# Optimization experiments

Measured on AMD Instinct MI355X. Metric: run time of the kernel, lower is better.

The kernel has to match this reference:

```python
import jax, jax.numpy as jnp
import numpy as np

N_EXPERTS = 8
TOP_K = 2


def setup_inputs() -> dict:
    key = jax.random.key(0)
    ks = jax.random.split(key, 5)
    B, T, C, E, H = 8, 2048, 256, 8, 682  # H = int(8/3*256)
    scale = 1.0 / np.sqrt(C)
    return {
        "x": jax.random.normal(ks[0], (B, T, C), dtype=jnp.float32),
        "router_w": jax.random.normal(ks[1], (E, C), dtype=jnp.float32) * scale,
        "w1": jax.random.normal(ks[2], (E, H, C), dtype=jnp.float32) * scale,
        "w2": jax.random.normal(ks[3], (E, C, H), dtype=jnp.float32) * (1.0 / np.sqrt(H)),
        "w3": jax.random.normal(ks[4], (E, H, C), dtype=jnp.float32) * scale,
    }


def reference(x, router_w, w1, w2, w3):
    B, T, C = x.shape
    flat = x.reshape(-1, C)  # [N, C]

    # Router: softmax over experts, top-k selection, renormalize.
    logits = flat @ router_w.T                     # [N, E]
    probs = jax.nn.softmax(logits, axis=-1)
    topk_probs, topk_idx = jax.lax.top_k(probs, TOP_K)
    topk_probs = topk_probs / (jnp.sum(topk_probs, axis=-1, keepdims=True) + 1e-9)

    # Dense gate matrix [N, E]: zero for non-selected experts (same math as
    # the masked loop, since unselected experts contribute weight 0).
    onehot = jax.nn.one_hot(topk_idx, N_EXPERTS, dtype=flat.dtype)  # [N, K, E]
    gates = jnp.einsum("nk,nke->ne", topk_probs, onehot)           # [N, E]

    # SwiGLU experts, computed densely over E and combined with gates.
    h1 = jnp.einsum("nc,ehc->neh", flat, w1)       # [N, E, H]
    h3 = jnp.einsum("nc,ehc->neh", flat, w3)       # [N, E, H]
    h = jax.nn.silu(h1) * h3                       # [N, E, H]
    y = jnp.einsum("neh,ech->nec", h, w2)          # [N, E, C]
    out = jnp.einsum("ne,nec->nc", gates, y)       # [N, C]
    return out.reshape(B, T, C)
```

## Files before the change

kernel.cpp:

```cpp
#include <hip/hip_runtime.h>
#include <hip/hip_bf16.h>

#define N_TOK 16384
#define C_DIM 256
#define E_NUM 8
#define H_DIM 682
#define H_PAD 768
#define NROWS (N_TOK * 2)
#define HB 64
#define APB (NROWS / HB)

typedef short short8 __attribute__((ext_vector_type(8)));
typedef float floatx4 __attribute__((ext_vector_type(4)));
typedef unsigned int uint;

__device__ inline unsigned short f2bf(float v) {
    union { float f; uint u; } x; x.f = v;
    uint r = (x.u + 0x7fffu + ((x.u >> 16) & 1u)) >> 16;
    return (unsigned short)r;
}
__device__ inline float bf2f(unsigned short v) {
    union { uint u; float f; } x; x.u = ((uint)v) << 16; return x.f;
}

__device__ __forceinline__ void load_lds16(const void* g, void* l) {
    __builtin_amdgcn_global_load_lds(
        (const __attribute__((address_space(1))) unsigned int*)g,
        (__attribute__((address_space(3))) unsigned int*)l, 16, 0, 0);
}

#define P13 (E_NUM * H_PAD * (C_DIM / 2))
#define P2  (E_NUM * C_DIM * (H_PAD / 2))
__global__ void wconvert(const float* __restrict__ w1, const float* __restrict__ w3,
                         const float* __restrict__ w2, unsigned short* __restrict__ w1b,
                         unsigned short* __restrict__ w3b, unsigned short* __restrict__ w2b) {
    int idx = blockIdx.x * 256 + threadIdx.x;
    if (idx < 2 * P13) {
        const float* src = (idx < P13) ? w1 : w3;
        unsigned short* dst = (idx < P13) ? w1b : w3b;
        int i = (idx < P13) ? idx : idx - P13;
        int e = i / (H_PAD * (C_DIM / 2));
        int rem = i - e * (H_PAD * (C_DIM / 2));
        int r = rem / (C_DIM / 2);
        int c2 = rem - r * (C_DIM / 2);
        uint v = 0;
        if (r < H_DIM) {
            const float2 f = *(const float2*)(src + ((size_t)e * H_DIM + r) * C_DIM + c2 * 2);
            v = (uint)f2bf(f.x) | ((uint)f2bf(f.y) << 16);
        }
        ((uint*)dst)[i] = v;
    } else if (idx < 2 * P13 + P2) {
        int i = idx - 2 * P13;
        int e = i / (C_DIM * (H_PAD / 2));
        int rem = i - e * (C_DIM * (H_PAD / 2));
        int r = rem / (H_PAD / 2);
        int c2 = rem - r * (H_PAD / 2);
        uint v = 0;
        if (c2 * 2 < H_DIM) {
            const float2 f = *(const float2*)(w2 + ((size_t)e * C_DIM + r) * H_DIM + c2 * 2);
            v = (uint)f2bf(f.x) | ((uint)f2bf(f.y) << 16);
        }
        ((uint*)w2b)[i] = v;
    }
}

__global__ __launch_bounds__(256) void router_kernel(
    const float* __restrict__ x, const float* __restrict__ rw,
    unsigned short* __restrict__ xb, int* __restrict__ as_e, float* __restrict__ as_gate) {
    __shared__ float rws[E_NUM * C_DIM];
    int tid = threadIdx.x;
    for (int i = tid; i < E_NUM * C_DIM; i += 256) rws[i] = rw[i];
    __syncthreads();
    int wave = tid >> 6, lane = tid & 63;
    int t = blockIdx.x * 4 + wave;
    const float4 xv = *(const float4*)(x + (size_t)t * C_DIM + lane * 4);
    uint2 pk;
    pk.x = (uint)f2bf(xv.x) | ((uint)f2bf(xv.y) << 16);
    pk.y = (uint)f2bf(xv.z) | ((uint)f2bf(xv.w) << 16);
    *(uint2*)(xb + (size_t)t * C_DIM + lane * 4) = pk;
    float p[E_NUM];
#pragma unroll
    for (int e = 0; e < E_NUM; e++) {
        const float* wr = &rws[e * C_DIM + lane * 4];
        p[e] = xv.x * wr[0] + xv.y * wr[1] + xv.z * wr[2] + xv.w * wr[3];
    }
#pragma unroll
    for (int off = 32; off >= 1; off >>= 1) {
#pragma unroll
        for (int e = 0; e < E_NUM; e++) p[e] += __shfl_down(p[e], off, 64);
    }
    if (lane == 0) {
        float m = p[0];
#pragma unroll
        for (int e = 1; e < E_NUM; e++) m = fmaxf(m, p[e]);
        float s = 0.f, q[E_NUM];
#pragma unroll
        for (int e = 0; e < E_NUM; e++) { q[e] = expf(p[e] - m); s += q[e]; }
#pragma unroll
        for (int e = 0; e < E_NUM; e++) q[e] /= s;
        int e0 = 0;
#pragma unroll
        for (int e = 1; e < E_NUM; e++) if (q[e] > q[e0]) e0 = e;
        int e1 = (e0 == 0) ? 1 : 0;
#pragma unroll
        for (int e = 0; e < E_NUM; e++) {
            if (e != e0 && q[e] > q[e1]) e1 = e;
        }
        float g0 = q[e0], g1 = q[e1];
        float denom = g0 + g1 + 1e-9f;
        g0 /= denom; g1 /= denom;
        as_e[t * 2] = e0; as_gate[t * 2] = g0;
        as_e[t * 2 + 1] = e1; as_gate[t * 2 + 1] = g1;
    }
}

__global__ __launch_bounds__(256) void hist_kernel(const int* __restrict__ as_e,
                                                   int* __restrict__ block_hist) {
    __shared__ int lh[E_NUM];
    int b = blockIdx.x, tid = threadIdx.x;
    if (tid < E_NUM) lh[tid] = 0;
    __syncthreads();
    for (int i = tid; i < APB; i += 256) atomicAdd(&lh[as_e[b * APB + i]], 1);
    __syncthreads();
    if (tid < E_NUM) block_hist[b * E_NUM + tid] = lh[tid];
}

__global__ void scan2_kernel(const int* __restrict__ block_hist, int* __restrict__ offsets,
                             int* __restrict__ block_base) {
    __shared__ int tot[E_NUM], off[E_NUM];
    int e = threadIdx.x;
    if (e < E_NUM) {
        int s = 0;
        for (int b = 0; b < HB; b++) s += block_hist[b * E_NUM + e];
        tot[e] = s;
    }
    __syncthreads();
    if (e == 0) {
        int acc = 0;
        for (int i = 0; i < E_NUM; i++) { off[i] = acc; offsets[i] = acc; acc += tot[i]; }
        offsets[E_NUM] = acc;
    }
    __syncthreads();
    if (e < E_NUM) {
        int acc = off[e];
        for (int b = 0; b < HB; b++) { block_base[b * E_NUM + e] = acc; acc += block_hist[b * E_NUM + e]; }
    }
}

__global__ __launch_bounds__(256) void scatter_kernel(
    const int* __restrict__ as_e, const int* __restrict__ block_base,
    int* __restrict__ row_token, int* __restrict__ as_row) {
    __shared__ int cur[E_NUM];
    int b = blockIdx.x, tid = threadIdx.x;
    if (tid < E_NUM) cur[tid] = block_base[b * E_NUM + tid];
    __syncthreads();
    for (int i = tid; i < APB; i += 256) {
        int a = b * APB + i;
        int e = as_e[a];
        int p = atomicAdd(&cur[e], 1);
        row_token[p] = a >> 1;
        as_row[a] = p;
    }
}

__global__ __launch_bounds__(256, 2) void expert_ffn1(
    const unsigned short* __restrict__ xb, const unsigned short* __restrict__ w1b,
    const unsigned short* __restrict__ w3b, const int* __restrict__ offsets,
    const int* __restrict__ row_token, unsigned short* __restrict__ h) {
    int e = blockIdx.x >> 6;
    int mt = blockIdx.x & 63;
    int c = blockIdx.y;
    int off0 = offsets[e], off1 = offsets[e + 1];
    int row0 = off0 + mt * 128;
    if (row0 >= off1) return;
    int mval = min(128, off1 - row0);

    __shared__ union {
        struct { unsigned short A[128 * 32], B1[128 * 32], B3[128 * 32]; } s;
        unsigned short Hs[128 * 136];
    } sm;

    int tid = threadIdx.x, lane = tid & 63, w = tid >> 6;
    int wm = w & 1, wn = w >> 1;
    int ra = tid >> 2;
    int acol = (tid & 3) * 8;
    int tok0 = row_token[row0 + min(ra, mval - 1)];
    int tok1 = row_token[row0 + min(ra + 64, mval - 1)];
    const unsigned short* a0p = xb + (size_t)tok0 * C_DIM + acol;
    const unsigned short* a1p = xb + (size_t)tok1 * C_DIM + acol;
    const unsigned short* b1p0 = w1b + ((size_t)e * H_PAD + c * 128 + ra) * C_DIM + acol;
    const unsigned short* b1p1 = b1p0 + (size_t)64 * C_DIM;
    const unsigned short* b3p0 = w3b + ((size_t)e * H_PAD + c * 128 + ra) * C_DIM + acol;
    const unsigned short* b3p1 = b3p0 + (size_t)64 * C_DIM;

    unsigned short* ldsA0 = sm.s.A + w * 512;
    unsigned short* ldsA1 = sm.s.A + 2048 + w * 512;
    unsigned short* ldsB10 = sm.s.B1 + w * 512;
    unsigned short* ldsB11 = sm.s.B1 + 2048 + w * 512;
    unsigned short* ldsB30 = sm.s.B3 + w * 512;
    unsigned short* ldsB31 = sm.s.B3 + 2048 + w * 512;

    int ko = (lane >> 4) * 8;
    int l15 = lane & 15;
    int arowf = wm * 64 + l15;
    int browf = wn * 64 + l15;
    int quad = lane >> 4;

    floatx4 acc1[4][4], acc3[4][4];
#pragma unroll
    for (int m = 0; m < 4; m++)
#pragma unroll
        for (int n = 0; n < 4; n++) {
            acc1[m][n] = (floatx4){0.f, 0.f, 0.f, 0.f};
            acc3[m][n] = (floatx4){0.f, 0.f, 0.f, 0.f};
        }

    for (int kt = 0; kt < 8; kt++) {
        int kb = kt * 32;
        load_lds16(a0p + kb, ldsA0);
        load_lds16(a1p + kb, ldsA1);
        load_lds16(b1p0 + kb, ldsB10);
        load_lds16(b1p1 + kb, ldsB11);
        load_lds16(b3p0 + kb, ldsB30);
        load_lds16(b3p1 + kb, ldsB31);
        __syncthreads();
        short8 af[4], b1f[4], b3f[4];
#pragma unroll
        for (int m = 0; m < 4; m++) af[m] = *(short8*)&sm.s.A[(arowf + m * 16) * 32 + ko];
#pragma unroll
        for (int n = 0; n < 4; n++) {
            b1f[n] = *(short8*)&sm.s.B1[(browf + n * 16) * 32 + ko];
            b3f[n] = *(short8*)&sm.s.B3[(browf + n * 16) * 32 + ko];
        }
#pragma unroll
        for (int m = 0; m < 4; m++)
#pragma unroll
            for (int n = 0; n < 4; n++) {
                acc1[m][n] = __builtin_amdgcn_mfma_f32_16x16x32_bf16(af[m], b1f[n], acc1[m][n], 0, 0, 0);
                acc3[m][n] = __builtin_amdgcn_mfma_f32_16x16x32_bf16(af[m], b3f[n], acc3[m][n], 0, 0, 0);
            }
        __syncthreads();
    }

#pragma unroll
    for (int m = 0; m < 4; m++)
#pragma unroll
        for (int n = 0; n < 4; n++)
#pragma unroll
            for (int r = 0; r < 4; r++) {
                float h1 = acc1[m][n][r], h3 = acc3[m][n][r];
                float sv = h1 / (1.0f + __expf(-h1)) * h3;
                sm.Hs[(wm * 64 + m * 16 + quad * 4 + r) * 136 + wn * 64 + n * 16 + l15] = f2bf(sv);
            }
    __syncthreads();
#pragma unroll
    for (int it = 0; it < 8; it++) {
        int s = it * 256 + tid;
        int row = s >> 4, c16 = s & 15;
        if (row < mval)
            *(int4*)(h + (size_t)(row0 + row) * H_PAD + c * 128 + c16 * 8) =
                *(int4*)&sm.Hs[row * 136 + c16 * 8];
    }
}

__global__ __launch_bounds__(256, 2) void expert_ffn2(
    const unsigned short* __restrict__ h, const unsigned short* __restrict__ w2b,
    const int* __restrict__ offsets, unsigned short* __restrict__ y) {
    int e = blockIdx.x >> 6;
    int mt = blockIdx.x & 63;
    int p = blockIdx.y;
    int off0 = offsets[e], off1 = offsets[e + 1];
    int row0 = off0 + mt * 128;
    if (row0 >= off1) return;
    int mval = min(128, off1 - row0);

    __shared__ union {
        struct { unsigned short A[128 * 32], B[128 * 32]; } s;
        unsigned short Hs[128 * 136];
    } sm;

    int tid = threadIdx.x, lane = tid & 63, w = tid >> 6;
    int wm = w & 1, wn = w >> 1;
    int ra = tid >> 2;
    int acol = (tid & 3) * 8;
    const unsigned short* ap0 = h + (size_t)(row0 + ra) * H_PAD + acol;
    const unsigned short* ap1 = ap0 + (size_t)64 * H_PAD;
    const unsigned short* bp0 = w2b + ((size_t)e * C_DIM + p * 128 + ra) * H_PAD + acol;
    const unsigned short* bp1 = bp0 + (size_t)64 * H_PAD;

    unsigned short* ldsA0 = sm.s.A + w * 512;
    unsigned short* ldsA1 = sm.s.A + 2048 + w * 512;
    unsigned short* ldsB0 = sm.s.B + w * 512;
    unsigned short* ldsB1 = sm.s.B + 2048 + w * 512;

    floatx4 acc[4][4];
#pragma unroll
    for (int m = 0; m < 4; m++)
#pragma unroll
        for (int n = 0; n < 4; n++) acc[m][n] = (floatx4){0.f, 0.f, 0.f, 0.f};

    int ko = (lane >> 4) * 8;
    int l15 = lane & 15;
    int arowf = wm * 64 + l15;
    int browf = wn * 64 + l15;
    int quad = lane >> 4;

    for (int kt = 0; kt < H_PAD / 32; kt++) {
        int kb = kt * 32;
        load_lds16(ap0 + kb, ldsA0);
        load_lds16(ap1 + kb, ldsA1);
        load_lds16(bp0 + kb, ldsB0);
        load_lds16(bp1 + kb, ldsB1);
        __syncthreads();
        short8 af[4], bf[4];
#pragma unroll
        for (int m = 0; m < 4; m++) af[m] = *(short8*)&sm.s.A[(arowf + m * 16) * 32 + ko];
#pragma unroll
        for (int n = 0; n < 4; n++) bf[n] = *(short8*)&sm.s.B[(browf + n * 16) * 32 + ko];
#pragma unroll
        for (int m = 0; m < 4; m++)
#pragma unroll
            for (int n = 0; n < 4; n++)
                acc[m][n] = __builtin_amdgcn_mfma_f32_16x16x32_bf16(af[m], bf[n], acc[m][n], 0, 0, 0);
        __syncthreads();
    }

#pragma unroll
    for (int m = 0; m < 4; m++)
#pragma unroll
        for (int n = 0; n < 4; n++)
#pragma unroll
            for (int r = 0; r < 4; r++)
                sm.Hs[(wm * 64 + m * 16 + quad * 4 + r) * 136 + wn * 64 + n * 16 + l15] =
                    f2bf(acc[m][n][r]);
    __syncthreads();
#pragma unroll
    for (int it = 0; it < 8; it++) {
        int s = it * 256 + tid;
        int row = s >> 4, c16 = s & 15;
        if (row < mval)
            *(int4*)(y + (size_t)(row0 + row) * C_DIM + p * 128 + c16 * 8) =
                *(int4*)&sm.Hs[row * 136 + c16 * 8];
    }
}

__global__ __launch_bounds__(256) void combine_kernel(
    const unsigned short* __restrict__ y, const int* __restrict__ as_row,
    const float* __restrict__ as_gate, float* __restrict__ out) {
    int tid = threadIdx.x, lane = tid & 63;
    int t = blockIdx.x * 4 + (tid >> 6);
    int r0 = as_row[2 * t], r1 = as_row[2 * t + 1];
    float g0 = as_gate[2 * t], g1 = as_gate[2 * t + 1];
    uint2 a = *(const uint2*)(y + (size_t)r0 * C_DIM + lane * 4);
    uint2 b = *(const uint2*)(y + (size_t)r1 * C_DIM + lane * 4);
    float4 o;
    o.x = g0 * bf2f((unsigned short)(a.x & 0xffff)) + g1 * bf2f((unsigned short)(b.x & 0xffff));
    o.y = g0 * bf2f((unsigned short)(a.x >> 16)) + g1 * bf2f((unsigned short)(b.x >> 16));
    o.z = g0 * bf2f((unsigned short)(a.y & 0xffff)) + g1 * bf2f((unsigned short)(b.y & 0xffff));
    o.w = g0 * bf2f((unsigned short)(a.y >> 16)) + g1 * bf2f((unsigned short)(b.y >> 16));
    *(float4*)(out + (size_t)t * C_DIM + lane * 4) = o;
}

extern "C" void kernel_launch(void* const* d_in, const int* in_sizes, int n_in,
                              void* d_out, int out_size, void* d_ws, size_t ws_size,
                              hipStream_t stream) {
    const float* x = (const float*)d_in[0];
    const float* rw = (const float*)d_in[1];
    const float* w1 = (const float*)d_in[2];
    const float* w2 = (const float*)d_in[3];
    const float* w3 = (const float*)d_in[4];
    float* out = (float*)d_out;

    char* ws = (char*)d_ws;
    size_t o = 0;
    auto alloc = [&](size_t bytes) {
        void* p = ws + o;
        o = (o + bytes + 255) & ~(size_t)255;
        return p;
    };
    unsigned short* xb = (unsigned short*)alloc((size_t)N_TOK * C_DIM * 2);
    unsigned short* w1b = (unsigned short*)alloc((size_t)E_NUM * H_PAD * C_DIM * 2);
    unsigned short* w3b = (unsigned short*)alloc((size_t)E_NUM * H_PAD * C_DIM * 2);
    unsigned short* w2b = (unsigned short*)alloc((size_t)E_NUM * C_DIM * H_PAD * 2);
    unsigned short* hbuf = (unsigned short*)alloc((size_t)(NROWS + 128) * H_PAD * 2);
    unsigned short* ybuf = (unsigned short*)alloc((size_t)NROWS * C_DIM * 2);
    int* offsets = (int*)alloc((E_NUM + 1) * 4);
    int* as_e = (int*)alloc(NROWS * 4);
    float* as_gate = (float*)alloc(NROWS * 4);
    int* row_token = (int*)alloc(NROWS * 4);
    int* as_row = (int*)alloc(NROWS * 4);
    int* block_hist = (int*)alloc(HB * E_NUM * 4);
    int* block_base = (int*)alloc(HB * E_NUM * 4);

    wconvert<<<(2 * P13 + P2 + 255) / 256, 256, 0, stream>>>(w1, w3, w2, w1b, w3b, w2b);
    router_kernel<<<N_TOK / 4, 256, 0, stream>>>(x, rw, xb, as_e, as_gate);
    hist_kernel<<<HB, 256, 0, stream>>>(as_e, block_hist);
    scan2_kernel<<<1, 64, 0, stream>>>(block_hist, offsets, block_base);
    scatter_kernel<<<HB, 256, 0, stream>>>(as_e, block_base, row_token, as_row);

    expert_ffn1<<<dim3(E_NUM * 64, 6), 256, 0, stream>>>(xb, w1b, w3b, offsets, row_token, hbuf);
    expert_ffn2<<<dim3(E_NUM * 64, 2), 256, 0, stream>>>(hbuf, w2b, offsets, ybuf);
    combine_kernel<<<N_TOK / 4, 256, 0, stream>>>(ybuf, as_row, as_gate, out);
}
```

Baseline: 207.6 us.

## Double-buffer LDS tiles in both expert FFN GEMM kernels

Both expert GEMM kernels now hold two LDS stages. Each iteration issues the global-to-LDS loads for the next K tile right after the barrier and then runs the MFMAs on the current tile. This drops one barrier per iteration and lets global memory latency overlap with matrix compute. The cost is doubled LDS for the staging buffers (48KB in ffn1), which could limit occupancy. The overlap is also lost if the compiler inserts conservative memory waits before the LDS reads.

```diff
diff --git a/kernel.cpp b/kernel.cpp
--- a/kernel.cpp
+++ b/kernel.cpp
@@ -176,7 +176,7 @@
     int mval = min(128, off1 - row0);
 
     __shared__ union {
-        struct { unsigned short A[128 * 32], B1[128 * 32], B3[128 * 32]; } s;
+        unsigned short buf[2][12288];
         unsigned short Hs[128 * 136];
     } sm;
 
@@ -193,12 +193,17 @@
     const unsigned short* b3p0 = w3b + ((size_t)e * H_PAD + c * 128 + ra) * C_DIM + acol;
     const unsigned short* b3p1 = b3p0 + (size_t)64 * C_DIM;
 
-    unsigned short* ldsA0 = sm.s.A + w * 512;
-    unsigned short* ldsA1 = sm.s.A + 2048 + w * 512;
-    unsigned short* ldsB10 = sm.s.B1 + w * 512;
-    unsigned short* ldsB11 = sm.s.B1 + 2048 + w * 512;
-    unsigned short* ldsB30 = sm.s.B3 + w * 512;
-    unsigned short* ldsB31 = sm.s.B3 + 2048 + w * 512;
+    int wofs = w * 512;
+    auto stage = [&](int kt, int s) {
+        int kb = kt * 32;
+        unsigned short* base = sm.buf[s];
+        load_lds16(a0p + kb, base + wofs);
+        load_lds16(a1p + kb, base + 2048 + wofs);
+        load_lds16(b1p0 + kb, base + 4096 + wofs);
+        load_lds16(b1p1 + kb, base + 6144 + wofs);
+        load_lds16(b3p0 + kb, base + 8192 + wofs);
+        load_lds16(b3p1 + kb, base + 10240 + wofs);
+    };
 
     int ko = (lane >> 4) * 8;
     int l15 = lane & 15;
@@ -206,6 +211,8 @@
     int browf = wn * 64 + l15;
     int quad = lane >> 4;
 
+    stage(0, 0);
+
     floatx4 acc1[4][4], acc3[4][4];
 #pragma unroll
     for (int m = 0; m < 4; m++)
@@ -216,21 +223,16 @@
         }
 
     for (int kt = 0; kt < 8; kt++) {
-        int kb = kt * 32;
-        load_lds16(a0p + kb, ldsA0);
-        load_lds16(a1p + kb, ldsA1);
-        load_lds16(b1p0 + kb, ldsB10);
-        load_lds16(b1p1 + kb, ldsB11);
-        load_lds16(b3p0 + kb, ldsB30);
-        load_lds16(b3p1 + kb, ldsB31);
         __syncthreads();
+        if (kt + 1 < 8) stage(kt + 1, (kt + 1) & 1);
+        const unsigned short* cur = sm.buf[kt & 1];
         short8 af[4], b1f[4], b3f[4];
 #pragma unroll
-        for (int m = 0; m < 4; m++) af[m] = *(short8*)&sm.s.A[(arowf + m * 16) * 32 + ko];
+        for (int m = 0; m < 4; m++) af[m] = *(short8*)&cur[(arowf + m * 16) * 32 + ko];
 #pragma unroll
         for (int n = 0; n < 4; n++) {
-            b1f[n] = *(short8*)&sm.s.B1[(browf + n * 16) * 32 + ko];
-            b3f[n] = *(short8*)&sm.s.B3[(browf + n * 16) * 32 + ko];
+            b1f[n] = *(short8*)&cur[4096 + (browf + n * 16) * 32 + ko];
+            b3f[n] = *(short8*)&cur[8192 + (browf + n * 16) * 32 + ko];
         }
 #pragma unroll
         for (int m = 0; m < 4; m++)
@@ -239,8 +241,8 @@
                 acc1[m][n] = __builtin_amdgcn_mfma_f32_16x16x32_bf16(af[m], b1f[n], acc1[m][n], 0, 0, 0);
                 acc3[m][n] = __builtin_amdgcn_mfma_f32_16x16x32_bf16(af[m], b3f[n], acc3[m][n], 0, 0, 0);
             }
-        __syncthreads();
-    }
+    }
+    __syncthreads();
 
 #pragma unroll
     for (int m = 0; m < 4; m++)
@@ -275,7 +277,7 @@
     int mval = min(128, off1 - row0);
 
     __shared__ union {
-        struct { unsigned short A[128 * 32], B[128 * 32]; } s;
+        unsigned short buf[2][8192];
         unsigned short Hs[128 * 136];
     } sm;
 
@@ -288,16 +290,15 @@
     const unsigned short* bp0 = w2b + ((size_t)e * C_DIM + p * 128 + ra) * H_PAD + acol;
     const unsigned short* bp1 = bp0 + (size_t)64 * H_PAD;
 
-    unsigned short* ldsA0 = sm.s.A + w * 512;
-    unsigned short* ldsA1 = sm.s.A + 2048 + w * 512;
-    unsigned short* ldsB0 = sm.s.B + w * 512;
-    unsigned short* ldsB1 = sm.s.B + 2048 + w * 512;
-
-    floatx4 acc[4][4];
-#pragma unroll
-    for (int m = 0; m < 4; m++)
-#pragma unroll
-        for (int n = 0; n < 4; n++) acc[m][n] = (floatx4){0.f, 0.f, 0.f, 0.f};
+    int wofs = w * 512;
+    auto stage = [&](int kt, int s) {
+        int kb = kt * 32;
+        unsigned short* base = sm.buf[s];
+        load_lds16(ap0 + kb, base + wofs);
+        load_lds16(ap1 + kb, base + 2048 + wofs);
+        load_lds16(bp0 + kb, base + 4096 + wofs);
+        load_lds16(bp1 + kb, base + 6144 + wofs);
+    };
 
     int ko = (lane >> 4) * 8;
     int l15 = lane & 15;
@@ -305,25 +306,30 @@
     int browf = wn * 64 + l15;
     int quad = lane >> 4;
 
+    stage(0, 0);
+
+    floatx4 acc[4][4];
+#pragma unroll
+    for (int m = 0; m < 4; m++)
+#pragma unroll
+        for (int n = 0; n < 4; n++) acc[m][n] = (floatx4){0.f, 0.f, 0.f, 0.f};
+
     for (int kt = 0; kt < H_PAD / 32; kt++) {
-        int kb = kt * 32;
-        load_lds16(ap0 + kb, ldsA0);
-        load_lds16(ap1 + kb, ldsA1);
-        load_lds16(bp0 + kb, ldsB0);
-        load_lds16(bp1 + kb, ldsB1);
         __syncthreads();
+        if (kt + 1 < H_PAD / 32) stage(kt + 1, (kt + 1) & 1);
+        const unsigned short* cur = sm.buf[kt & 1];
         short8 af[4], bf[4];
 #pragma unroll
-        for (int m = 0; m < 4; m++) af[m] = *(short8*)&sm.s.A[(arowf + m * 16) * 32 + ko];
-#pragma unroll
-        for (int n = 0; n < 4; n++) bf[n] = *(short8*)&sm.s.B[(browf + n * 16) * 32 + ko];
+        for (int m = 0; m < 4; m++) af[m] = *(short8*)&cur[(arowf + m * 16) * 32 + ko];
+#pragma unroll
+        for (int n = 0; n < 4; n++) bf[n] = *(short8*)&cur[4096 + (browf + n * 16) * 32 + ko];
 #pragma unroll
         for (int m = 0; m < 4; m++)
 #pragma unroll
             for (int n = 0; n < 4; n++)
                 acc[m][n] = __builtin_amdgcn_mfma_f32_16x16x32_bf16(af[m], bf[n], acc[m][n], 0, 0, 0);
-        __syncthreads();
-    }
+    }
+    __syncthreads();
 
 #pragma unroll
     for (int m = 0; m < 4; m++)
```

Result: faster. 198.7 us (-4.2%).
